# Performance work log

Hardware: AMD Instinct MI355X
Metric: run time of the kernel (lower is better)

Reference implementation:

```python
import jax, jax.numpy as jnp
import numpy as np

NUM_HEADS = 8
HEAD_DIM = 64
D_MODEL = NUM_HEADS * HEAD_DIM  # 512
B, T = 4, 2048


def setup_inputs() -> dict:
    key = jax.random.key(0)
    k1, k2 = jax.random.split(key)
    x = jax.random.normal(k1, (B, T, D_MODEL), dtype=jnp.float32)
    mask = jnp.ones((B, 1, T, T), dtype=jnp.float32)
    W = jax.random.normal(k2, (D_MODEL, 3 * D_MODEL), dtype=jnp.float32) * (D_MODEL ** -0.5)
    b = jnp.zeros((3 * D_MODEL,), dtype=jnp.float32)
    return {"x": x, "mask": mask, "W": W, "b": b}


def reference(x, mask, W, b):
    batch = x.shape[0]
    # fused QKV projection: [B, T, 3D]
    qkv = jnp.einsum("btd,de->bte", x, W) + b
    # NOTE: faithful to torch reshape [B, T, H, Hd, 3] -> the size-3 axis is innermost
    qkv = qkv.reshape(batch, -1, NUM_HEADS, HEAD_DIM, 3)
    qkv = jnp.transpose(qkv, (4, 0, 2, 1, 3))  # [3, B, H, T, Hd]
    q, k, v = qkv[0], qkv[1], qkv[2]
    logits = jnp.einsum("bhqd,bhkd->bhqk", q, k) / (HEAD_DIM ** 0.5)
    logits = logits + (1.0 - mask) * -10000.0
    w = jax.nn.softmax(logits, axis=-1)
    out = jnp.einsum("bhqk,bhkd->bhqd", w, v)  # [B, H, T, Hd]
    out = jnp.transpose(out, (0, 2, 1, 3)).reshape(batch, -1, NUM_HEADS * HEAD_DIM)
    return out
```

## Files before the change

### kernel.cpp

```cpp
#include <hip/hip_runtime.h>
#include <hip/hip_bf16.h>
#include <stdint.h>

#define B_   4
#define T_   2048
#define H_   8
#define HD_  64
#define DM_  512
#define N3_  1536

typedef short bf_el;
typedef __attribute__((ext_vector_type(8))) bf_el bfrag;
typedef __attribute__((ext_vector_type(4))) bf_el bfrag4;
typedef __attribute__((ext_vector_type(4))) float ffrag;

#define SCALE_L2E  0.18033688011112043f
#define MASK_L2E   14426.950408889634f

static __device__ __forceinline__ unsigned short f2bf(float f) {
    union { float f; unsigned int i; } v; v.f = f;
    unsigned int r = v.i + 0x7fff + ((v.i >> 16) & 1);
    return (unsigned short)(r >> 16);
}
static __device__ __forceinline__ unsigned short f2bf_fast(float f) {
    union { float f; unsigned int i; } v; v.f = f;
    return (unsigned short)((v.i + 0x8000u) >> 16);
}

__global__ __launch_bounds__(256) void k_prep(const float* __restrict__ W,
                                              const float* __restrict__ X,
                                              const float* __restrict__ mask,
                                              unsigned short* __restrict__ Wt,
                                              unsigned short* __restrict__ Xb,
                                              int* __restrict__ flags) {
    __shared__ __align__(16) unsigned short Ls[64 * 72];
    const int bid = blockIdx.x;
    const int tid = threadIdx.x;

    if (bid < 512) {
        const int R0 = bid * 16;
        const int mb = R0 >> 11;
        const int q0 = R0 & 2047;
        const int e  = mb * 32 + (q0 >> 6);
        const int wave = tid >> 6, lane = tid & 63;
        unsigned int acc = 0u;
        const float* base = mask + (size_t)R0 * T_ + tid * 8;
#pragma unroll
        for (int rr = 0; rr < 16; ++rr) {
            const uint4 u0 = *(const uint4*)(base + (size_t)rr * T_);
            const uint4 u1 = *(const uint4*)(base + (size_t)rr * T_ + 4);
            acc |= (u0.x ^ 0x3F800000u) | (u0.y ^ 0x3F800000u) |
                   (u0.z ^ 0x3F800000u) | (u0.w ^ 0x3F800000u) |
                   (u1.x ^ 0x3F800000u) | (u1.y ^ 0x3F800000u) |
                   (u1.z ^ 0x3F800000u) | (u1.w ^ 0x3F800000u);
        }
        unsigned long long bal = __ballot(acc != 0u);
        if (lane == 0 && bal != 0ULL) {
#pragma unroll
            for (int j = 0; j < 8; ++j)
                if ((bal >> (8 * j)) & 0xFFULL)
                    atomicOr(&flags[e * 32 + wave * 8 + j], 1);
        }
        return;
    }
    if (bid < 768) {
        const int b2 = bid - 512;
        const float* src = X + (size_t)b2 * 16384;
        unsigned short* dst = Xb + (size_t)b2 * 16384;
#pragma unroll
        for (int j = 0; j < 8; ++j) {
            int idx = j * 512 + tid * 2;
            float4 f0 = *(const float4*)(src + idx * 4);
            float4 f1 = *(const float4*)(src + idx * 4 + 4);
            __align__(16) unsigned short t8[8];
            t8[0] = f2bf_fast(f0.x); t8[1] = f2bf_fast(f0.y);
            t8[2] = f2bf_fast(f0.z); t8[3] = f2bf_fast(f0.w);
            t8[4] = f2bf_fast(f1.x); t8[5] = f2bf_fast(f1.y);
            t8[6] = f2bf_fast(f1.z); t8[7] = f2bf_fast(f1.w);
            *(uint4*)(dst + idx * 4) = *(const uint4*)t8;
        }
        return;
    }
    {
        const int t  = bid - 768;
        const int n0 = (t % 24) * 64;
        const int k0 = (t / 24) * 64;
#pragma unroll
        for (int i = 0; i < 4; ++i) {
            int chunk = tid + i * 256;
            int k = chunk >> 4;
            int c = chunk & 15;
            float4 f = *(const float4*)(W + (size_t)(k0 + k) * N3_ + n0 + c * 4);
            unsigned short* p = Ls + k * 72 + c * 4;
            p[0] = f2bf(f.x); p[1] = f2bf(f.y); p[2] = f2bf(f.z); p[3] = f2bf(f.w);
        }
        __syncthreads();
        const int n = tid >> 2;
        const int g = tid & 3;
        __align__(16) unsigned short tmp[16];
#pragma unroll
        for (int i = 0; i < 16; ++i) tmp[i] = Ls[(g * 16 + i) * 72 + n];
        uint4* dst = (uint4*)(Wt + (size_t)(n0 + n) * DM_ + k0 + g * 16);
        dst[0] = *(const uint4*)(tmp);
        dst[1] = *(const uint4*)(tmp + 8);
    }
}

__global__ __launch_bounds__(256, 4) void k_gemm_qkv(const unsigned short* __restrict__ Xb,
                                                     const unsigned short* __restrict__ Wt,
                                                     const float* __restrict__ bias,
                                                     unsigned short* __restrict__ Qb,
                                                     unsigned short* __restrict__ Kb,
                                                     unsigned short* __restrict__ Vtb) {
    __shared__ __align__(16) unsigned short SH[12800];
    unsigned short* As = SH;
    unsigned short* Bs = SH + 2560;
    unsigned short* Cs = SH;

    const int tid  = threadIdx.x;
    const int wave = tid >> 6;
    const int lane = tid & 63;
    const int quad = lane >> 4;
    const int l16  = lane & 15;
    const int wm = wave >> 1, wn = wave & 1;
    const int h  = blockIdx.x >> 7;
    const int m0 = (blockIdx.x & 127) * 64;
    const int n0 = h * 192;

    float bvv[6];
#pragma unroll
    for (int ni = 0; ni < 6; ++ni) bvv[ni] = bias[n0 + wn * 96 + ni * 16 + l16];

    ffrag acc[2][6];
#pragma unroll
    for (int i = 0; i < 2; ++i)
#pragma unroll
        for (int j = 0; j < 6; ++j) acc[i][j] = (ffrag){0.f, 0.f, 0.f, 0.f};

    const int ar = tid >> 2, ac = tid & 3;
    const int br0 = tid >> 2, br1 = (tid + 256) >> 2, br2 = (tid + 512) >> 2;
    const int bc  = tid & 3;
    uint4 pa, pb0, pb1, pb2;

    pa  = *(const uint4*)(Xb + (size_t)(m0 + ar) * DM_ + ac * 8);
    pb0 = *(const uint4*)(Wt + (size_t)(n0 + br0) * DM_ + bc * 8);
    pb1 = *(const uint4*)(Wt + (size_t)(n0 + br1) * DM_ + bc * 8);
    pb2 = *(const uint4*)(Wt + (size_t)(n0 + br2) * DM_ + bc * 8);

    for (int kt = 0; kt < 16; ++kt) {
        __syncthreads();
        *(uint4*)(As + ar * 40 + ac * 8)  = pa;
        *(uint4*)(Bs + br0 * 40 + bc * 8) = pb0;
        *(uint4*)(Bs + br1 * 40 + bc * 8) = pb1;
        *(uint4*)(Bs + br2 * 40 + bc * 8) = pb2;
        __syncthreads();
        if (kt < 15) {
            const int ko = (kt + 1) * 32;
            pa  = *(const uint4*)(Xb + (size_t)(m0 + ar) * DM_ + ko + ac * 8);
            pb0 = *(const uint4*)(Wt + (size_t)(n0 + br0) * DM_ + ko + bc * 8);
            pb1 = *(const uint4*)(Wt + (size_t)(n0 + br1) * DM_ + ko + bc * 8);
            pb2 = *(const uint4*)(Wt + (size_t)(n0 + br2) * DM_ + ko + bc * 8);
        }
        bfrag af[2], bfr[6];
#pragma unroll
        for (int mi = 0; mi < 2; ++mi)
            af[mi] = *(const bfrag*)(As + (wm * 32 + mi * 16 + l16) * 40 + quad * 8);
#pragma unroll
        for (int ni = 0; ni < 6; ++ni)
            bfr[ni] = *(const bfrag*)(Bs + (wn * 96 + ni * 16 + l16) * 40 + quad * 8);
#pragma unroll
        for (int mi = 0; mi < 2; ++mi)
#pragma unroll
            for (int ni = 0; ni < 6; ++ni)
                acc[mi][ni] = __builtin_amdgcn_mfma_f32_16x16x32_bf16(af[mi], bfr[ni], acc[mi][ni], 0, 0, 0);
    }

    const int b  = m0 >> 11;
    const int tb = m0 & 2047;
    const size_t bh = (size_t)(b * 8 + h);
    float cscale[6];
#pragma unroll
    for (int ni = 0; ni < 6; ++ni) {
        int c = wn * 96 + ni * 16 + l16;
        cscale[ni] = (c % 3 == 0) ? SCALE_L2E : 1.0f;
    }
    __syncthreads();
#pragma unroll
    for (int mi = 0; mi < 2; ++mi)
#pragma unroll
        for (int ni = 0; ni < 6; ++ni)
#pragma unroll
            for (int reg = 0; reg < 4; ++reg) {
                int r = wm * 32 + mi * 16 + quad * 4 + reg;
                int c = wn * 96 + ni * 16 + l16;
                Cs[r * 200 + c] = f2bf_fast((acc[mi][ni][reg] + bvv[ni]) * cscale[ni]);
            }
    __syncthreads();
#pragma unroll
    for (int i = 0; i < 2; ++i) {
        int idx = tid + i * 256;
        int tl = idx >> 3, hc = (idx & 7) * 8;
        __align__(16) unsigned short tq[8], tk[8];
#pragma unroll
        for (int j = 0; j < 8; ++j) {
            tq[j] = Cs[tl * 200 + (hc + j) * 3 + 0];
            tk[j] = Cs[tl * 200 + (hc + j) * 3 + 1];
        }
        *(uint4*)(Qb + (bh * T_ + tb + tl) * HD_ + hc) = *(const uint4*)tq;
        *(uint4*)(Kb + (bh * T_ + tb + tl) * HD_ + hc) = *(const uint4*)tk;
    }
#pragma unroll
    for (int i = 0; i < 2; ++i) {
        int idx = tid + i * 256;
        int hd = idx >> 3, t8 = (idx & 7) * 8;
        __align__(16) unsigned short tv[8];
#pragma unroll
        for (int j = 0; j < 8; ++j)
            tv[j] = Cs[(t8 + j) * 200 + hd * 3 + 2];
        *(uint4*)(Vtb + (bh * HD_ + hd) * T_ + tb + t8) = *(const uint4*)tv;
    }
}

__global__ __launch_bounds__(256) void k_attn(const unsigned short* __restrict__ Q,
                                              const unsigned short* __restrict__ K,
                                              const unsigned short* __restrict__ Vt,
                                              const float* __restrict__ mask,
                                              const int* __restrict__ flags,
                                              float* __restrict__ out) {
    __shared__ __align__(16) unsigned short Ks[64 * 72];
    __shared__ __align__(16) unsigned short Vs[64 * 72];

    const int tid = threadIdx.x;
    const int wave = tid >> 6, lane = tid & 63;
    const int quad = lane >> 4, l16 = lane & 15;
    const int bh = blockIdx.x & 31, b = bh >> 3, h = bh & 7;
    const int qt = blockIdx.x >> 5;
    const int q0 = qt * 64;
    const int fbase = (b * 32 + qt) * 32;
    const int q = q0 + wave * 16 + l16;

    bfrag qf[2];
    {
        size_t qrow = ((size_t)bh * T_ + q) * HD_;
        qf[0] = *(const bfrag*)(Q + qrow + quad * 8);
        qf[1] = *(const bfrag*)(Q + qrow + 32 + quad * 8);
    }
    float lsum = 0.f;
    ffrag of[4];
#pragma unroll
    for (int dt = 0; dt < 4; ++dt) of[dt] = (ffrag){0.f, 0.f, 0.f, 0.f};

    const int sr0 = tid >> 3, sr1 = (tid + 256) >> 3, sc = tid & 7;
    const unsigned short* Kbase = K  + (size_t)bh * T_ * HD_;
    const unsigned short* Vbase = Vt + (size_t)bh * HD_ * T_;
    const float* mq = mask + ((size_t)b * T_ + q) * T_;

    for (int kt = 0; kt < 32; ++kt) {
        __syncthreads();
        {
            const int kn = kt * 64;
            *(uint4*)(Ks + sr0 * 72 + sc * 8) =
                *(const uint4*)(Kbase + (size_t)(kn + sr0) * HD_ + sc * 8);
            *(uint4*)(Ks + sr1 * 72 + sc * 8) =
                *(const uint4*)(Kbase + (size_t)(kn + sr1) * HD_ + sc * 8);
            *(uint4*)(Vs + sr0 * 72 + sc * 8) =
                *(const uint4*)(Vbase + (size_t)sr0 * T_ + kn + sc * 8);
            *(uint4*)(Vs + sr1 * 72 + sc * 8) =
                *(const uint4*)(Vbase + (size_t)sr1 * T_ + kn + sc * 8);
        }
        const int fl = flags[fbase + kt];
        __syncthreads();
#pragma unroll
        for (int ns = 0; ns < 4; ++ns) {
            ffrag a = (ffrag){0.f, 0.f, 0.f, 0.f};
#pragma unroll
            for (int ks = 0; ks < 2; ++ks) {
                bfrag kf = *(const bfrag*)(Ks + (ns * 16 + l16) * 72 + (ks * 4 + quad) * 8);
                a = __builtin_amdgcn_mfma_f32_16x16x32_bf16(kf, qf[ks], a, 0, 0, 0);
            }
            bfrag4 pf;
            if (fl) {
                const float* mp = mq + kt * 64 + ns * 16 + quad * 4;
#pragma unroll
                for (int reg = 0; reg < 4; ++reg) {
                    float p = __builtin_amdgcn_exp2f(
                        fmaf(mp[reg], MASK_L2E, a[reg] - MASK_L2E));
                    lsum += p;
                    pf[reg] = (bf_el)f2bf_fast(p);
                }
            } else {
#pragma unroll
                for (int reg = 0; reg < 4; ++reg) {
                    float p = __builtin_amdgcn_exp2f(a[reg]);
                    lsum += p;
                    pf[reg] = (bf_el)f2bf_fast(p);
                }
            }
#pragma unroll
            for (int dt = 0; dt < 4; ++dt) {
                bfrag4 vf = *(const bfrag4*)(Vs + (dt * 16 + l16) * 72 + ns * 16 + quad * 4);
                of[dt] = __builtin_amdgcn_mfma_f32_16x16x16bf16_1k(vf, pf, of[dt], 0, 0, 0);
            }
        }
    }
    float s = lsum;
    s += __shfl_xor(s, 16, 64);
    s += __shfl_xor(s, 32, 64);
    const float inv = 1.0f / s;
    float* orow = out + ((size_t)b * T_ + q) * DM_ + h * 64;
#pragma unroll
    for (int dt = 0; dt < 4; ++dt) {
        float4 v;
        v.x = of[dt][0] * inv; v.y = of[dt][1] * inv;
        v.z = of[dt][2] * inv; v.w = of[dt][3] * inv;
        *(float4*)(orow + dt * 16 + quad * 4) = v;
    }
}

extern "C" void kernel_launch(void* const* d_in, const int* in_sizes, int n_in,
                              void* d_out, int out_size, void* d_ws, size_t ws_size,
                              hipStream_t stream) {
    const float* X    = (const float*)d_in[0];
    const float* mask = (const float*)d_in[1];
    const float* W    = (const float*)d_in[2];
    const float* bias = (const float*)d_in[3];
    float* outp = (float*)d_out;

    char* ws = (char*)d_ws;
    unsigned short* Wt  = (unsigned short*)(ws);
    unsigned short* Xb  = (unsigned short*)(ws + 1572864);
    unsigned short* Qb  = (unsigned short*)(ws + 9961472);
    unsigned short* Kb  = (unsigned short*)(ws + 18350080);
    unsigned short* Vtb = (unsigned short*)(ws + 26738688);
    int*            flg = (int*)(ws + 35127296);

    hipMemsetAsync(flg, 0, 16384, stream);
    k_prep     <<<dim3(960),  256, 0, stream>>>(W, X, mask, Wt, Xb, flg);
    k_gemm_qkv <<<dim3(1024), 256, 0, stream>>>(Xb, Wt, bias, Qb, Kb, Vtb);
    k_attn     <<<dim3(1024), 256, 0, stream>>>(Qb, Kb, Vtb, mask, flg, outp);
}
```

Before: 222.8 us.

## Overlap mask scan with QKV GEMM, use global mask flag, double-buffer K/V

The mask-scan blocks move out of the prep kernel and are interleaved with the QKV GEMM blocks (one scan block per two GEMM blocks), so the mask read overlaps GEMM compute. The per-tile flags become a single global any-mask flag. The attention kernel double-buffers K/V in shared memory with register prefetch of the next tile, which removes one barrier per iteration. The cost is coarser masking: any non-one mask element forces the slow masked path on every tile. Shared memory use also doubles, which may lower occupancy.

Result: no change. 218.8 us (-1.8%).

```diff
diff --git a/kernel.cpp b/kernel.cpp
--- a/kernel.cpp
+++ b/kernel.cpp
@@ -29,44 +29,15 @@
 
 __global__ __launch_bounds__(256) void k_prep(const float* __restrict__ W,
                                               const float* __restrict__ X,
-                                              const float* __restrict__ mask,
                                               unsigned short* __restrict__ Wt,
-                                              unsigned short* __restrict__ Xb,
-                                              int* __restrict__ flags) {
+                                              unsigned short* __restrict__ Xb) {
     __shared__ __align__(16) unsigned short Ls[64 * 72];
     const int bid = blockIdx.x;
     const int tid = threadIdx.x;
 
-    if (bid < 512) {
-        const int R0 = bid * 16;
-        const int mb = R0 >> 11;
-        const int q0 = R0 & 2047;
-        const int e  = mb * 32 + (q0 >> 6);
-        const int wave = tid >> 6, lane = tid & 63;
-        unsigned int acc = 0u;
-        const float* base = mask + (size_t)R0 * T_ + tid * 8;
-#pragma unroll
-        for (int rr = 0; rr < 16; ++rr) {
-            const uint4 u0 = *(const uint4*)(base + (size_t)rr * T_);
-            const uint4 u1 = *(const uint4*)(base + (size_t)rr * T_ + 4);
-            acc |= (u0.x ^ 0x3F800000u) | (u0.y ^ 0x3F800000u) |
-                   (u0.z ^ 0x3F800000u) | (u0.w ^ 0x3F800000u) |
-                   (u1.x ^ 0x3F800000u) | (u1.y ^ 0x3F800000u) |
-                   (u1.z ^ 0x3F800000u) | (u1.w ^ 0x3F800000u);
-        }
-        unsigned long long bal = __ballot(acc != 0u);
-        if (lane == 0 && bal != 0ULL) {
-#pragma unroll
-            for (int j = 0; j < 8; ++j)
-                if ((bal >> (8 * j)) & 0xFFULL)
-                    atomicOr(&flags[e * 32 + wave * 8 + j], 1);
-        }
-        return;
-    }
-    if (bid < 768) {
-        const int b2 = bid - 512;
-        const float* src = X + (size_t)b2 * 16384;
-        unsigned short* dst = Xb + (size_t)b2 * 16384;
+    if (bid < 256) {
+        const float* src = X + (size_t)bid * 16384;
+        unsigned short* dst = Xb + (size_t)bid * 16384;
 #pragma unroll
         for (int j = 0; j < 8; ++j) {
             int idx = j * 512 + tid * 2;
@@ -82,7 +53,7 @@
         return;
     }
     {
-        const int t  = bid - 768;
+        const int t  = bid - 256;
         const int n0 = (t % 24) * 64;
         const int k0 = (t / 24) * 64;
 #pragma unroll
@@ -109,22 +80,46 @@
 __global__ __launch_bounds__(256, 4) void k_gemm_qkv(const unsigned short* __restrict__ Xb,
                                                      const unsigned short* __restrict__ Wt,
                                                      const float* __restrict__ bias,
+                                                     const float* __restrict__ mask,
+                                                     int* __restrict__ anymask,
                                                      unsigned short* __restrict__ Qb,
                                                      unsigned short* __restrict__ Kb,
                                                      unsigned short* __restrict__ Vtb) {
     __shared__ __align__(16) unsigned short SH[12800];
+    const int tid = threadIdx.x;
+    const int g3  = blockIdx.x / 3;
+    const int r3  = blockIdx.x - g3 * 3;
+
+    if (r3 == 2) {
+        const int R0 = g3 * 16;
+        unsigned int acc = 0u;
+        const float* base = mask + (size_t)R0 * T_ + tid * 8;
+#pragma unroll
+        for (int rr = 0; rr < 16; ++rr) {
+            const uint4 u0 = *(const uint4*)(base + (size_t)rr * T_);
+            const uint4 u1 = *(const uint4*)(base + (size_t)rr * T_ + 4);
+            acc |= (u0.x ^ 0x3F800000u) | (u0.y ^ 0x3F800000u) |
+                   (u0.z ^ 0x3F800000u) | (u0.w ^ 0x3F800000u) |
+                   (u1.x ^ 0x3F800000u) | (u1.y ^ 0x3F800000u) |
+                   (u1.z ^ 0x3F800000u) | (u1.w ^ 0x3F800000u);
+        }
+        unsigned long long bal = __ballot(acc != 0u);
+        if ((tid & 63) == 0 && bal != 0ULL) atomicOr(anymask, 1);
+        return;
+    }
+
     unsigned short* As = SH;
     unsigned short* Bs = SH + 2560;
     unsigned short* Cs = SH;
 
-    const int tid  = threadIdx.x;
+    const int gemm_id = g3 * 2 + r3;
     const int wave = tid >> 6;
     const int lane = tid & 63;
     const int quad = lane >> 4;
     const int l16  = lane & 15;
     const int wm = wave >> 1, wn = wave & 1;
-    const int h  = blockIdx.x >> 7;
-    const int m0 = (blockIdx.x & 127) * 64;
+    const int h  = gemm_id >> 7;
+    const int m0 = (gemm_id & 127) * 64;
     const int n0 = h * 192;
 
     float bvv[6];
@@ -225,10 +220,10 @@
                                               const unsigned short* __restrict__ K,
                                               const unsigned short* __restrict__ Vt,
                                               const float* __restrict__ mask,
-                                              const int* __restrict__ flags,
+                                              const int* __restrict__ anymask,
                                               float* __restrict__ out) {
-    __shared__ __align__(16) unsigned short Ks[64 * 72];
-    __shared__ __align__(16) unsigned short Vs[64 * 72];
+    __shared__ __align__(16) unsigned short Ks[2][64 * 72];
+    __shared__ __align__(16) unsigned short Vs[2][64 * 72];
 
     const int tid = threadIdx.x;
     const int wave = tid >> 6, lane = tid & 63;
@@ -236,8 +231,9 @@
     const int bh = blockIdx.x & 31, b = bh >> 3, h = bh & 7;
     const int qt = blockIdx.x >> 5;
     const int q0 = qt * 64;
-    const int fbase = (b * 32 + qt) * 32;
     const int q = q0 + wave * 16 + l16;
+
+    const int gmask = anymask[0];
 
     bfrag qf[2];
     {
@@ -255,31 +251,36 @@
     const unsigned short* Vbase = Vt + (size_t)bh * HD_ * T_;
     const float* mq = mask + ((size_t)b * T_ + q) * T_;
 
+    uint4 kreg[2], vreg[2];
+    kreg[0] = *(const uint4*)(Kbase + (size_t)sr0 * HD_ + sc * 8);
+    kreg[1] = *(const uint4*)(Kbase + (size_t)sr1 * HD_ + sc * 8);
+    vreg[0] = *(const uint4*)(Vbase + (size_t)sr0 * T_ + sc * 8);
+    vreg[1] = *(const uint4*)(Vbase + (size_t)sr1 * T_ + sc * 8);
+    *(uint4*)(&Ks[0][sr0 * 72 + sc * 8]) = kreg[0];
+    *(uint4*)(&Ks[0][sr1 * 72 + sc * 8]) = kreg[1];
+    *(uint4*)(&Vs[0][sr0 * 72 + sc * 8]) = vreg[0];
+    *(uint4*)(&Vs[0][sr1 * 72 + sc * 8]) = vreg[1];
+    __syncthreads();
+
     for (int kt = 0; kt < 32; ++kt) {
-        __syncthreads();
-        {
-            const int kn = kt * 64;
-            *(uint4*)(Ks + sr0 * 72 + sc * 8) =
-                *(const uint4*)(Kbase + (size_t)(kn + sr0) * HD_ + sc * 8);
-            *(uint4*)(Ks + sr1 * 72 + sc * 8) =
-                *(const uint4*)(Kbase + (size_t)(kn + sr1) * HD_ + sc * 8);
-            *(uint4*)(Vs + sr0 * 72 + sc * 8) =
-                *(const uint4*)(Vbase + (size_t)sr0 * T_ + kn + sc * 8);
-            *(uint4*)(Vs + sr1 * 72 + sc * 8) =
-                *(const uint4*)(Vbase + (size_t)sr1 * T_ + kn + sc * 8);
-        }
-        const int fl = flags[fbase + kt];
-        __syncthreads();
+        const int cur = kt & 1;
+        if (kt < 31) {
+            const int kn = (kt + 1) * 64;
+            kreg[0] = *(const uint4*)(Kbase + (size_t)(kn + sr0) * HD_ + sc * 8);
+            kreg[1] = *(const uint4*)(Kbase + (size_t)(kn + sr1) * HD_ + sc * 8);
+            vreg[0] = *(const uint4*)(Vbase + (size_t)sr0 * T_ + kn + sc * 8);
+            vreg[1] = *(const uint4*)(Vbase + (size_t)sr1 * T_ + kn + sc * 8);
+        }
 #pragma unroll
         for (int ns = 0; ns < 4; ++ns) {
             ffrag a = (ffrag){0.f, 0.f, 0.f, 0.f};
 #pragma unroll
             for (int ks = 0; ks < 2; ++ks) {
-                bfrag kf = *(const bfrag*)(Ks + (ns * 16 + l16) * 72 + (ks * 4 + quad) * 8);
+                bfrag kf = *(const bfrag*)(&Ks[cur][(ns * 16 + l16) * 72 + (ks * 4 + quad) * 8]);
                 a = __builtin_amdgcn_mfma_f32_16x16x32_bf16(kf, qf[ks], a, 0, 0, 0);
             }
             bfrag4 pf;
-            if (fl) {
+            if (gmask) {
                 const float* mp = mq + kt * 64 + ns * 16 + quad * 4;
 #pragma unroll
                 for (int reg = 0; reg < 4; ++reg) {
@@ -298,9 +299,17 @@
             }
 #pragma unroll
             for (int dt = 0; dt < 4; ++dt) {
-                bfrag4 vf = *(const bfrag4*)(Vs + (dt * 16 + l16) * 72 + ns * 16 + quad * 4);
+                bfrag4 vf = *(const bfrag4*)(&Vs[cur][(dt * 16 + l16) * 72 + ns * 16 + quad * 4]);
                 of[dt] = __builtin_amdgcn_mfma_f32_16x16x16bf16_1k(vf, pf, of[dt], 0, 0, 0);
             }
+        }
+        if (kt < 31) {
+            const int nxt = cur ^ 1;
+            *(uint4*)(&Ks[nxt][sr0 * 72 + sc * 8]) = kreg[0];
+            *(uint4*)(&Ks[nxt][sr1 * 72 + sc * 8]) = kreg[1];
+            *(uint4*)(&Vs[nxt][sr0 * 72 + sc * 8]) = vreg[0];
+            *(uint4*)(&Vs[nxt][sr1 * 72 + sc * 8]) = vreg[1];
+            __syncthreads();
         }
     }
     float s = lsum;
@@ -334,8 +343,8 @@
     unsigned short* Vtb = (unsigned short*)(ws + 26738688);
     int*            flg = (int*)(ws + 35127296);
 
-    hipMemsetAsync(flg, 0, 16384, stream);
-    k_prep     <<<dim3(960),  256, 0, stream>>>(W, X, mask, Wt, Xb, flg);
-    k_gemm_qkv <<<dim3(1024), 256, 0, stream>>>(Xb, Wt, bias, Qb, Kb, Vtb);
+    hipMemsetAsync(flg, 0, 4, stream);
+    k_prep     <<<dim3(448),  256, 0, stream>>>(W, X, Wt, Xb);
+    k_gemm_qkv <<<dim3(1536), 256, 0, stream>>>(Xb, Wt, bias, mask, flg, Qb, Kb, Vtb);
     k_attn     <<<dim3(1024), 256, 0, stream>>>(Qb, Kb, Vtb, mask, flg, outp);
 }
```
